# Performance work log

Hardware: AMD Instinct MI355X
Metric: run time of the kernel (lower is better)

## Reference

```python
import jax, jax.numpy as jnp
import numpy as np

TAU = 1.0

def setup_inputs() -> dict:
    key = jax.random.key(0)
    k1, k2 = jax.random.split(key)
    x = jax.random.uniform(k1, (1, 8192), dtype=jnp.float32)
    weight = jax.random.uniform(k2, (8192, 8192), dtype=jnp.float32)  # uniform_(0,1) init
    t = 128
    return {"x": x, "weight": weight, "t": t}

def reference(x, weight, t):
    # x = x / max(x) * 255 ; x = floor(x / tau)
    xq = jnp.floor((x / jnp.max(x)) * 255.0 / TAU)
    # spike mask: int32(t) == int32(x[0][i]) per element, vectorized
    spikes = (xq[0].astype(jnp.int32) == jnp.int32(t)).astype(weight.dtype)  # [in_features]
    # broadcast multiply: [out_features, in_features] * [in_features]
    return weight * spikes
```

## Files before the change

kernel.cpp:

```cpp
#include <hip/hip_runtime.h>

#define N_COLS 8192
#define LOG2_COLS 13

__global__ __launch_bounds__(1024) void spike_kernel(const float* __restrict__ x,
                                                     const int* __restrict__ t_ptr,
                                                     int* __restrict__ meta) {
    __shared__ float smax[16];
    __shared__ float s_maxv;
    __shared__ int s_count;
    const int tid = threadIdx.x;

    if (tid == 0) s_count = 0;

    float vals[8];
    float m = -1e30f;
#pragma unroll
    for (int j = 0; j < 8; ++j) {
        vals[j] = x[tid + j * 1024];
        m = fmaxf(m, vals[j]);
    }
#pragma unroll
    for (int off = 32; off > 0; off >>= 1)
        m = fmaxf(m, __shfl_down(m, off, 64));
    if ((tid & 63) == 0) smax[tid >> 6] = m;
    __syncthreads();
    if (tid < 16) {
        float mm = smax[tid];
#pragma unroll
        for (int off = 8; off > 0; off >>= 1)
            mm = fmaxf(mm, __shfl_down(mm, off, 16));
        if (tid == 0) s_maxv = mm;
    }
    __syncthreads();

    const float maxv = s_maxv;
    const int t = *t_ptr;
#pragma unroll
    for (int j = 0; j < 8; ++j) {
        const int q = (int)floorf((vals[j] / maxv) * 255.0f);
        if (q == t) {
            const int slot = atomicAdd(&s_count, 1);
            meta[1 + slot] = tid + j * 1024;
        }
    }
    __syncthreads();
    if (tid == 0) meta[0] = s_count;
}

__global__ __launch_bounds__(256) void scatter_kernel(const float* __restrict__ w,
                                                      const int* __restrict__ meta,
                                                      float* __restrict__ out) {
    const int count = meta[0];
    const int* cols = meta + 1;
    const long total = (long)count << LOG2_COLS;
    const long stride = (long)gridDim.x * blockDim.x;
    for (long idx = (long)blockIdx.x * blockDim.x + threadIdx.x; idx < total;
         idx += stride) {
        const int k = (int)(idx >> LOG2_COLS);
        const int r = (int)(idx & (N_COLS - 1));
        const long off = ((long)r << LOG2_COLS) + cols[k];
        out[off] = w[off];
    }
}

extern "C" void kernel_launch(void* const* d_in, const int* in_sizes, int n_in,
                              void* d_out, int out_size, void* d_ws, size_t ws_size,
                              hipStream_t stream) {
    const float* x = (const float*)d_in[0];
    const float* w = (const float*)d_in[1];
    const int* t = (const int*)d_in[2];
    float* out = (float*)d_out;
    int* meta = (int*)d_ws;

    spike_kernel<<<1, 1024, 0, stream>>>(x, t, meta);

    hipMemsetAsync(out, 0, (size_t)out_size, stream);

    scatter_kernel<<<2048, 256, 0, stream>>>(w, meta, out);
}
```

Before: 390.1 us.

## Fuse spike detection into scatter kernel, recomputing column list per block

Removes the single-block spike kernel and the global metadata round-trip. Each of 256 blocks now reads x with vector loads, reduces the max, builds the list of spiking columns in shared memory, and then copies its own 32 rows of those columns from weight to out. This drops one kernel launch and its serialisation, but every block redundantly reads x and computes the max. The memset of the 256 MB output still dominates, so the expected effect is small.

```diff
diff --git a/kernel.cpp b/kernel.cpp
--- a/kernel.cpp
+++ b/kernel.cpp
@@ -1,65 +1,54 @@
 #include <hip/hip_runtime.h>
 
 #define N_COLS 8192
-#define LOG2_COLS 13
 
-__global__ __launch_bounds__(1024) void spike_kernel(const float* __restrict__ x,
-                                                     const int* __restrict__ t_ptr,
-                                                     int* __restrict__ meta) {
-    __shared__ float smax[16];
-    __shared__ float s_maxv;
+typedef float floatx4 __attribute__((ext_vector_type(4)));
+
+__global__ __launch_bounds__(256) void fused_scatter_kernel(
+        const float* __restrict__ x, const float* __restrict__ w,
+        const int* __restrict__ t_ptr, float* __restrict__ out) {
+    __shared__ int s_cols[N_COLS];
+    __shared__ float s_wmax[4];
     __shared__ int s_count;
     const int tid = threadIdx.x;
-
     if (tid == 0) s_count = 0;
 
-    float vals[8];
+    const floatx4* __restrict__ x4 = (const floatx4*)x;
+    floatx4 xv[8];
     float m = -1e30f;
 #pragma unroll
-    for (int j = 0; j < 8; ++j) {
-        vals[j] = x[tid + j * 1024];
-        m = fmaxf(m, vals[j]);
+    for (int k = 0; k < 8; ++k) {
+        xv[k] = x4[tid + (k << 8)];
+        m = fmaxf(fmaxf(fmaxf(m, xv[k].x), fmaxf(xv[k].y, xv[k].z)), xv[k].w);
     }
 #pragma unroll
     for (int off = 32; off > 0; off >>= 1)
         m = fmaxf(m, __shfl_down(m, off, 64));
-    if ((tid & 63) == 0) smax[tid >> 6] = m;
+    if ((tid & 63) == 0) s_wmax[tid >> 6] = m;
     __syncthreads();
-    if (tid < 16) {
-        float mm = smax[tid];
-#pragma unroll
-        for (int off = 8; off > 0; off >>= 1)
-            mm = fmaxf(mm, __shfl_down(mm, off, 16));
-        if (tid == 0) s_maxv = mm;
-    }
-    __syncthreads();
+    const float maxv = fmaxf(fmaxf(s_wmax[0], s_wmax[1]),
+                             fmaxf(s_wmax[2], s_wmax[3]));
 
-    const float maxv = s_maxv;
     const int t = *t_ptr;
 #pragma unroll
-    for (int j = 0; j < 8; ++j) {
-        const int q = (int)floorf((vals[j] / maxv) * 255.0f);
-        if (q == t) {
-            const int slot = atomicAdd(&s_count, 1);
-            meta[1 + slot] = tid + j * 1024;
+    for (int k = 0; k < 8; ++k) {
+        const int c0 = (tid + (k << 8)) << 2;
+        const float v[4] = {xv[k].x, xv[k].y, xv[k].z, xv[k].w};
+#pragma unroll
+        for (int j = 0; j < 4; ++j) {
+            const int q = (int)floorf((v[j] / maxv) * 255.0f);
+            if (q == t) s_cols[atomicAdd(&s_count, 1)] = c0 + j;
         }
     }
     __syncthreads();
-    if (tid == 0) meta[0] = s_count;
-}
+    const int count = s_count;
+    const int r0 = (int)blockIdx.x << 5;
 
-__global__ __launch_bounds__(256) void scatter_kernel(const float* __restrict__ w,
-                                                      const int* __restrict__ meta,
-                                                      float* __restrict__ out) {
-    const int count = meta[0];
-    const int* cols = meta + 1;
-    const long total = (long)count << LOG2_COLS;
-    const long stride = (long)gridDim.x * blockDim.x;
-    for (long idx = (long)blockIdx.x * blockDim.x + threadIdx.x; idx < total;
-         idx += stride) {
-        const int k = (int)(idx >> LOG2_COLS);
-        const int r = (int)(idx & (N_COLS - 1));
-        const long off = ((long)r << LOG2_COLS) + cols[k];
+    const int pairs = count << 5;
+    for (int p = tid; p < pairs; p += 256) {
+        const int k = p >> 5;
+        const int r = r0 + (p & 31);
+        const long off = ((long)r << 13) + s_cols[k];
         out[off] = w[off];
     }
 }
@@ -71,11 +60,8 @@
     const float* w = (const float*)d_in[1];
     const int* t = (const int*)d_in[2];
     float* out = (float*)d_out;
-    int* meta = (int*)d_ws;
-
-    spike_kernel<<<1, 1024, 0, stream>>>(x, t, meta);
 
     hipMemsetAsync(out, 0, (size_t)out_size, stream);
 
-    scatter_kernel<<<2048, 256, 0, stream>>>(w, meta, out);
+    fused_scatter_kernel<<<256, 256, 0, stream>>>(x, w, t, out);
 }
```

New measurement: 387.6 us. About the same (-0.6%).
